# Optimization experiments

Measured on AMD Instinct MI355X. Metric: run time of the kernel, lower is better.

## Reference

```python
import jax, jax.numpy as jnp
import numpy as np
import math

BLOCK_SIZE = 512

def _block_attention(query, key, value):
    # query/key/value: [B, S, H, D]; block-wise attention with PER-BLOCK softmax
    # and normalizer accumulation, faithful to _ring_attention_single (causal, no dropout).
    B, S, H, D = query.shape
    bs = BLOCK_SIZE
    nb = S // bs
    scale = 1.0 / math.sqrt(D)
    neg = jnp.where(jnp.triu(jnp.ones((bs, bs), dtype=bool), 1), -jnp.inf, 0.0)  # strict-upper causal mask for diagonal block
    outs = []
    for i in range(nb):  # small fixed number of blocks (8)
        qb = query[:, i * bs:(i + 1) * bs]                      # [B, bs, H, D]
        kb = key[:, :(i + 1) * bs]                              # [B, (i+1)*bs, H, D]
        vb = value[:, :(i + 1) * bs].reshape(B, i + 1, bs, H, D)
        s = jnp.einsum('bqhd,bkhd->bhqk', qb, kb) * scale       # [B, H, bs, (i+1)*bs]
        s = s.reshape(B, H, bs, i + 1, bs)
        s = s.at[:, :, :, i, :].add(neg)                        # causal mask on diagonal block j == i
        p = jax.nn.softmax(s, axis=-1)                          # softmax PER kv block (faithful to source)
        o = jnp.einsum('bhqjk,bjkhd->bqhd', p, vb)              # accumulated block outputs
        norm = p.sum(axis=-1).sum(axis=-1)                      # [B, H, bs] accumulated normalizer (== i+1 per row)
        norm = jnp.clip(norm, 1e-6, None).transpose(0, 2, 1)[..., None]  # [B, bs, H, 1]
        outs.append(o / norm)
    return jnp.concatenate(outs, axis=1)  # [B, S, H, D]


def setup_inputs() -> dict:
    key = jax.random.key(0)
    k1, k2, k3 = jax.random.split(key, 3)
    shape = (2, 4096, 16, 128)
    return {
        'query': jax.random.normal(k1, shape, dtype=jnp.float32),
        'key': jax.random.normal(k2, shape, dtype=jnp.float32),
        'value': jax.random.normal(k3, shape, dtype=jnp.float32),
    }


def reference(query, key, value):
    return _block_attention(query, key, value)
```

## Files before the change

### kernel.cpp

```cpp
#include <hip/hip_runtime.h>

typedef short bf16x8 __attribute__((ext_vector_type(8)));
typedef short bf16x4 __attribute__((ext_vector_type(4)));
typedef float f32x4  __attribute__((ext_vector_type(4)));
typedef float f32x16 __attribute__((ext_vector_type(16)));
typedef unsigned int u32;
typedef u32 u32x4 __attribute__((ext_vector_type(4)));

#define SEQ 4096
#define NH  16
#define HD  128

__device__ __forceinline__ short bf16_rne(float x) {
  u32 u = __builtin_bit_cast(u32, x);
  u = (u + 0x7FFFu + ((u >> 16) & 1u)) >> 16;
  return (short)u;
}

typedef __attribute__((address_space(1))) const void as1c_void;
typedef __attribute__((address_space(3))) void as3_void;

#define CVTPK(d, a, b) asm("v_cvt_pk_bf16_f32 %0, %1, %2" : "=v"(d) : "v"(a), "v"(b))
#define PLSWAP(x, y)   asm("v_permlane32_swap_b32 %0, %1" : "+v"(x), "+v"(y))

__global__ __launch_bounds__(256) void prep_k(const float* __restrict__ K,
                                              short* __restrict__ Kp) {
  int idx = blockIdx.x * 256 + threadIdx.x;
  int d4 = idx & 31;
  int s  = (idx >> 5) & 4095;
  int h  = (idx >> 17) & 15;
  int b  = idx >> 21;
  f32x4 v = *(const f32x4*)(K + (((size_t)(b * SEQ + s) * NH + h) << 7) + d4 * 4);
  bf16x4 o;
  o[0] = bf16_rne(v[0]); o[1] = bf16_rne(v[1]);
  o[2] = bf16_rne(v[2]); o[3] = bf16_rne(v[3]);
  int x = (d4 * 4) ^ ((s & 7) << 3);
  *(bf16x4*)(Kp + (((size_t)(b * NH + h) * SEQ + s) << 7) + x) = o;
}

__global__ __launch_bounds__(256) void prep_v(const float* __restrict__ V,
                                              short* __restrict__ Vt) {
  __shared__ short tile[64 * 128];
  int bid = blockIdx.x;
  int sb = bid & 63;
  int h  = (bid >> 6) & 15;
  int b  = bid >> 10;
  int t = threadIdx.x;
  {
    int s = t >> 2;
    int dbase = (t & 3) * 32;
    const float* src = V + (((size_t)(b * SEQ + sb * 64 + s) * NH + h) << 7) + dbase;
    int sw = (s & 7) << 3;
#pragma unroll
    for (int j = 0; j < 8; ++j) {
      f32x4 v = *(const f32x4*)(src + j * 4);
      bf16x4 o;
      o[0] = bf16_rne(v[0]); o[1] = bf16_rne(v[1]);
      o[2] = bf16_rne(v[2]); o[3] = bf16_rne(v[3]);
      int d = dbase + j * 4;
      *(bf16x4*)&tile[s * 128 + (d ^ sw)] = o;
    }
  }
  __syncthreads();
  {
    int w = t >> 6, l = t & 63, g = l >> 4, lq = l & 15;
    int srel = lq * 4;
#pragma unroll
    for (int j = 0; j < 8; ++j) {
      int d = w * 32 + j * 4 + g;
      bf16x4 o;
#pragma unroll
      for (int i = 0; i < 4; ++i) {
        int s = srel + i;
        o[i] = tile[s * 128 + (d ^ ((s & 7) << 3))];
      }
      int sp = srel ^ ((d & 7) << 3);
      *(bf16x4*)(Vt + (((size_t)(b * NH + h) * HD + d) << 12) + sb * 64 + sp) = o;
    }
  }
}

__global__ __launch_bounds__(256, 2) void attn_main(const float* __restrict__ Q,
                                                    const short* __restrict__ Kp,
                                                    const short* __restrict__ Vt,
                                                    float* __restrict__ Out) {
  __shared__ __align__(16) short sK[2][64 * 128];
  __shared__ __align__(16) short sV[2][128 * 64];

  int bid0 = (int)blockIdx.x;
  int bid = (bid0 & 7) * 64 + (bid0 >> 3);
  int p  = bid & 15;
  int h  = (bid >> 4) & 15;
  int b  = bid >> 8;

  int tid = threadIdx.x;
  int l = tid & 63, w = tid >> 6;
  int q5 = l & 31;
  int hi = l >> 5;
  int hi4 = hi * 4, hi8 = hi * 8;
  int cswz = (l & 7) << 4;

  int kcol[8], vcol[4];
#pragma unroll
  for (int i = 0; i < 8; ++i) kcol[i] = (i * 32 + hi * 16) ^ cswz;
#pragma unroll
  for (int ks = 0; ks < 4; ++ks) vcol[ks] = (ks * 32 + hi * 16) ^ cswz;

  const int pat[16] = {0,1,2,3, 8,9,10,11, 16,17,18,19, 24,25,26,27};

  const char* KbB = (const char*)(Kp + ((size_t)(b * NH + h) << 19));
  const char* VbB = (const char*)(Vt + ((size_t)(b * NH + h) << 19));

  const char* kgb[4]; const char* vgb[4]; int ldo[4];
#pragma unroll
  for (int j = 0; j < 4; ++j) {
    int idx = j * 256 + tid;
    kgb[j] = KbB + idx * 16;
    vgb[j] = VbB + (size_t)(idx >> 3) * 8192 + (idx & 7) * 16;
    ldo[j] = idx * 16;
  }

  const float SCL = 0.08838834764831845f * 1.4426950408889634f;

  for (int ts = 0; ts < 2; ++ts) {
    int qt = ts ? p : (31 - p);
    int iblk = qt >> 2;
    int qrow0 = qt * 128 + w * 32;
    int qg = qrow0 + q5;
    int qgrel = (qt & 3) * 128 + w * 32 + q5;
    int nch_w = (qt & 3) * 2 + (w >> 1) + 1;
    int ntot = 8 * iblk + (qt & 3) * 2 + 2;

    bf16x8 qf[8];
    {
      const float* qp = Q + (((size_t)(b * SEQ + qg) * NH + h) << 7);
#pragma unroll
      for (int i = 0; i < 8; ++i) {
        int d0 = i * 16 + hi8;
        f32x4 a = *(const f32x4*)(qp + d0);
        f32x4 c2 = *(const f32x4*)(qp + d0 + 4);
        bf16x8 f;
        f[0] = bf16_rne(a[0] * SCL);  f[1] = bf16_rne(a[1] * SCL);
        f[2] = bf16_rne(a[2] * SCL);  f[3] = bf16_rne(a[3] * SCL);
        f[4] = bf16_rne(c2[0] * SCL); f[5] = bf16_rne(c2[1] * SCL);
        f[6] = bf16_rne(c2[2] * SCL); f[7] = bf16_rne(c2[3] * SCL);
        qf[i] = f;
      }
    }

    f32x16 ot[4], ob[4];
#pragma unroll
    for (int dt = 0; dt < 4; ++dt) {
#pragma unroll
      for (int r = 0; r < 16; ++r) { ot[dt][r] = 0.f; ob[dt][r] = 0.f; }
    }
    float Z = 0.0f;

    __syncthreads();
#pragma unroll
    for (int j = 0; j < 4; ++j) {
      __builtin_amdgcn_global_load_lds((as1c_void*)kgb[j], (as3_void*)((char*)sK[0] + ldo[j]), 16, 0, 0);
      __builtin_amdgcn_global_load_lds((as1c_void*)vgb[j], (as3_void*)((char*)sV[0] + ldo[j]), 16, 0, 0);
    }

#pragma unroll 2
    for (int t = 0; t < ntot; ++t) {
      __syncthreads();

      if (t + 1 < ntot) {
        int bi = (t + 1) & 1;
#pragma unroll
        for (int j = 0; j < 4; ++j) {
          __builtin_amdgcn_global_load_lds((as1c_void*)(kgb[j] + (size_t)(t + 1) * 16384),
                                           (as3_void*)((char*)sK[bi] + ldo[j]), 16, 0, 0);
          __builtin_amdgcn_global_load_lds((as1c_void*)(vgb[j] + (size_t)(t + 1) * 128),
                                           (as3_void*)((char*)sV[bi] + ldo[j]), 16, 0, 0);
        }
      }

      int jb = t >> 3, c = t & 7;
      const int diag = (jb == iblk);

      if (!(diag && c >= nch_w)) {
        const char* kbuf = (const char*)sK[t & 1];
        const char* vbuf = (const char*)sV[t & 1];
        bf16x8 pa[4];
        float csum = 0.0f;

#pragma unroll
        for (int kt = 0; kt < 2; ++kt) {
          f32x16 st;
#pragma unroll
          for (int r = 0; r < 16; ++r) st[r] = 0.f;
          int rowb = kt * 8192 + q5 * 256;
          __builtin_amdgcn_s_setprio(1);
#pragma unroll
          for (int i = 0; i < 8; ++i) {
            bf16x8 kf = *(const bf16x8*)(kbuf + rowb + kcol[i]);
            st = __builtin_amdgcn_mfma_f32_32x32x16_bf16(kf, qf[i], st, 0, 0, 0);
          }
          __builtin_amdgcn_s_setprio(0);

          if (diag && c == nch_w - 1) {
            int lim = qgrel - (c * 64 + kt * 32);
#pragma unroll
            for (int r = 0; r < 16; ++r) {
              if (pat[r] + hi4 > lim) st[r] = -1e30f;
            }
          }

          float pr[16];
#pragma unroll
          for (int r = 0; r < 16; ++r) {
            pr[r] = __builtin_amdgcn_exp2f(st[r]);
            csum += pr[r];
          }
          u32 X0, X1, Y0, Y1;
          CVTPK(X0, pr[0], pr[1]); CVTPK(X1, pr[2], pr[3]);
          CVTPK(Y0, pr[4], pr[5]); CVTPK(Y1, pr[6], pr[7]);
          PLSWAP(X0, Y0); PLSWAP(X1, Y1);
          pa[kt * 2] = __builtin_bit_cast(bf16x8, (u32x4){X0, X1, Y0, Y1});
          u32 A0, A1, B0, B1;
          CVTPK(A0, pr[8], pr[9]);   CVTPK(A1, pr[10], pr[11]);
          CVTPK(B0, pr[12], pr[13]); CVTPK(B1, pr[14], pr[15]);
          PLSWAP(A0, B0); PLSWAP(A1, B1);
          pa[kt * 2 + 1] = __builtin_bit_cast(bf16x8, (u32x4){A0, A1, B0, B1});
        }
        Z += csum;

        __builtin_amdgcn_s_setprio(1);
#pragma unroll
        for (int ks = 0; ks < 4; ++ks) {
#pragma unroll
          for (int dt = 0; dt < 4; ++dt) {
            bf16x8 vf = *(const bf16x8*)(vbuf + (dt * 32 + q5) * 128 + vcol[ks]);
            ob[dt] = __builtin_amdgcn_mfma_f32_32x32x16_bf16(pa[ks], vf, ob[dt], 0, 0, 0);
          }
        }
        __builtin_amdgcn_s_setprio(0);
      }

      if ((t & 7) == 7 || t == ntot - 1) {
        float zf = Z + __shfl_xor(Z, 32, 64);
        float rz[16];
#pragma unroll
        for (int r = 0; r < 16; ++r) rz[r] = 1.0f / __shfl(zf, pat[r] + hi4, 64);
#pragma unroll
        for (int dt = 0; dt < 4; ++dt) {
#pragma unroll
          for (int r = 0; r < 16; ++r) {
            ot[dt][r] += ob[dt][r] * rz[r];
            ob[dt][r] = 0.f;
          }
        }
        Z = 0.0f;
      }
    }

    float rnorm = 1.0f / (float)(iblk + 1);
#pragma unroll
    for (int dt = 0; dt < 4; ++dt) {
#pragma unroll
      for (int r = 0; r < 16; ++r) {
        int qrow = qrow0 + pat[r] + hi4;
        Out[(((size_t)(b * SEQ + qrow) * NH + h) << 7) + dt * 32 + q5] = ot[dt][r] * rnorm;
      }
    }
  }
}

extern "C" void kernel_launch(void* const* d_in, const int* in_sizes, int n_in,
                              void* d_out, int out_size, void* d_ws, size_t ws_size,
                              hipStream_t stream) {
  const float* Q = (const float*)d_in[0];
  const float* K = (const float*)d_in[1];
  const float* V = (const float*)d_in[2];
  float* out = (float*)d_out;

  short* Kp = (short*)d_ws;
  short* Vt = Kp + (size_t)2 * NH * SEQ * HD;

  prep_k<<<(2 * NH * SEQ * (HD / 4)) / 256, 256, 0, stream>>>(K, Kp);
  prep_v<<<2 * NH * (SEQ / 64), 256, 0, stream>>>(V, Vt);
  attn_main<<<2 * NH * 16, 256, 0, stream>>>(Q, Kp, Vt, out);
}
```

Measured before the change: 212.1 us.

## Split V prefetch after QK MFMAs and interleave softmax with PV MFMAs

Issues the next tile's K load first and defers the V global-to-LDS load until after the QK^T MFMAs, spreading memory traffic across the iteration. Computes both 32-row score tiles up front, then interleaves the exp/convert of each half with its PV MFMAs, so VALU softmax work can overlap matrix-core work. Also computes the reciprocal once per lane before the shuffle instead of sixteen divides. The cost is higher register pressure from holding two score accumulators live at once.

```diff
diff --git a/kernel.cpp b/kernel.cpp
--- a/kernel.cpp
+++ b/kernel.cpp
@@ -167,15 +167,13 @@
     for (int t = 0; t < ntot; ++t) {
       __syncthreads();
 
-      if (t + 1 < ntot) {
-        int bi = (t + 1) & 1;
-#pragma unroll
-        for (int j = 0; j < 4; ++j) {
+      int bi = (t + 1) & 1;
+      const int more = (t + 1 < ntot);
+      if (more) {
+#pragma unroll
+        for (int j = 0; j < 4; ++j)
           __builtin_amdgcn_global_load_lds((as1c_void*)(kgb[j] + (size_t)(t + 1) * 16384),
                                            (as3_void*)((char*)sK[bi] + ldo[j]), 16, 0, 0);
-          __builtin_amdgcn_global_load_lds((as1c_void*)(vgb[j] + (size_t)(t + 1) * 128),
-                                           (as3_void*)((char*)sV[bi] + ldo[j]), 16, 0, 0);
-        }
       }
 
       int jb = t >> 3, c = t & 7;
@@ -184,67 +182,118 @@
       if (!(diag && c >= nch_w)) {
         const char* kbuf = (const char*)sK[t & 1];
         const char* vbuf = (const char*)sV[t & 1];
-        bf16x8 pa[4];
         float csum = 0.0f;
 
-#pragma unroll
-        for (int kt = 0; kt < 2; ++kt) {
-          f32x16 st;
-#pragma unroll
-          for (int r = 0; r < 16; ++r) st[r] = 0.f;
-          int rowb = kt * 8192 + q5 * 256;
-          __builtin_amdgcn_s_setprio(1);
-#pragma unroll
-          for (int i = 0; i < 8; ++i) {
-            bf16x8 kf = *(const bf16x8*)(kbuf + rowb + kcol[i]);
-            st = __builtin_amdgcn_mfma_f32_32x32x16_bf16(kf, qf[i], st, 0, 0, 0);
+        f32x16 st0, st1;
+#pragma unroll
+        for (int r = 0; r < 16; ++r) { st0[r] = 0.f; st1[r] = 0.f; }
+        int rowb = q5 * 256;
+        __builtin_amdgcn_s_setprio(1);
+#pragma unroll
+        for (int i = 0; i < 8; ++i) {
+          bf16x8 kf = *(const bf16x8*)(kbuf + rowb + kcol[i]);
+          st0 = __builtin_amdgcn_mfma_f32_32x32x16_bf16(kf, qf[i], st0, 0, 0, 0);
+        }
+#pragma unroll
+        for (int i = 0; i < 8; ++i) {
+          bf16x8 kf = *(const bf16x8*)(kbuf + 8192 + rowb + kcol[i]);
+          st1 = __builtin_amdgcn_mfma_f32_32x32x16_bf16(kf, qf[i], st1, 0, 0, 0);
+        }
+        __builtin_amdgcn_s_setprio(0);
+
+        if (more) {
+#pragma unroll
+          for (int j = 0; j < 4; ++j)
+            __builtin_amdgcn_global_load_lds((as1c_void*)(vgb[j] + (size_t)(t + 1) * 128),
+                                             (as3_void*)((char*)sV[bi] + ldo[j]), 16, 0, 0);
+        }
+
+        if (diag && c == nch_w - 1) {
+          int lim0 = qgrel - c * 64;
+          int lim1 = lim0 - 32;
+#pragma unroll
+          for (int r = 0; r < 16; ++r) {
+            int pr4 = pat[r] + hi4;
+            if (pr4 > lim0) st0[r] = -1e30f;
+            if (pr4 > lim1) st1[r] = -1e30f;
           }
-          __builtin_amdgcn_s_setprio(0);
-
-          if (diag && c == nch_w - 1) {
-            int lim = qgrel - (c * 64 + kt * 32);
-#pragma unroll
-            for (int r = 0; r < 16; ++r) {
-              if (pat[r] + hi4 > lim) st[r] = -1e30f;
-            }
-          }
-
+        }
+
+        bf16x8 pa0, pa1, pa2, pa3;
+        {
           float pr[16];
 #pragma unroll
           for (int r = 0; r < 16; ++r) {
-            pr[r] = __builtin_amdgcn_exp2f(st[r]);
+            pr[r] = __builtin_amdgcn_exp2f(st0[r]);
             csum += pr[r];
           }
-          u32 X0, X1, Y0, Y1;
-          CVTPK(X0, pr[0], pr[1]); CVTPK(X1, pr[2], pr[3]);
-          CVTPK(Y0, pr[4], pr[5]); CVTPK(Y1, pr[6], pr[7]);
+          u32 X0, X1, Y0, Y1, A0, A1, B0, B1;
+          CVTPK(X0, pr[0], pr[1]);   CVTPK(X1, pr[2], pr[3]);
+          CVTPK(Y0, pr[4], pr[5]);   CVTPK(Y1, pr[6], pr[7]);
           PLSWAP(X0, Y0); PLSWAP(X1, Y1);
-          pa[kt * 2] = __builtin_bit_cast(bf16x8, (u32x4){X0, X1, Y0, Y1});
-          u32 A0, A1, B0, B1;
+          pa0 = __builtin_bit_cast(bf16x8, (u32x4){X0, X1, Y0, Y1});
           CVTPK(A0, pr[8], pr[9]);   CVTPK(A1, pr[10], pr[11]);
           CVTPK(B0, pr[12], pr[13]); CVTPK(B1, pr[14], pr[15]);
           PLSWAP(A0, B0); PLSWAP(A1, B1);
-          pa[kt * 2 + 1] = __builtin_bit_cast(bf16x8, (u32x4){A0, A1, B0, B1});
-        }
+          pa1 = __builtin_bit_cast(bf16x8, (u32x4){A0, A1, B0, B1});
+        }
+        __builtin_amdgcn_s_setprio(1);
+#pragma unroll
+        for (int dt = 0; dt < 4; ++dt) {
+          bf16x8 vf = *(const bf16x8*)(vbuf + (dt * 32 + q5) * 128 + vcol[0]);
+          ob[dt] = __builtin_amdgcn_mfma_f32_32x32x16_bf16(pa0, vf, ob[dt], 0, 0, 0);
+        }
+#pragma unroll
+        for (int dt = 0; dt < 4; ++dt) {
+          bf16x8 vf = *(const bf16x8*)(vbuf + (dt * 32 + q5) * 128 + vcol[1]);
+          ob[dt] = __builtin_amdgcn_mfma_f32_32x32x16_bf16(pa1, vf, ob[dt], 0, 0, 0);
+        }
+        __builtin_amdgcn_s_setprio(0);
+
+        {
+          float pr[16];
+#pragma unroll
+          for (int r = 0; r < 16; ++r) {
+            pr[r] = __builtin_amdgcn_exp2f(st1[r]);
+            csum += pr[r];
+          }
+          u32 X0, X1, Y0, Y1, A0, A1, B0, B1;
+          CVTPK(X0, pr[0], pr[1]);   CVTPK(X1, pr[2], pr[3]);
+          CVTPK(Y0, pr[4], pr[5]);   CVTPK(Y1, pr[6], pr[7]);
+          PLSWAP(X0, Y0); PLSWAP(X1, Y1);
+          pa2 = __builtin_bit_cast(bf16x8, (u32x4){X0, X1, Y0, Y1});
+          CVTPK(A0, pr[8], pr[9]);   CVTPK(A1, pr[10], pr[11]);
+          CVTPK(B0, pr[12], pr[13]); CVTPK(B1, pr[14], pr[15]);
+          PLSWAP(A0, B0); PLSWAP(A1, B1);
+          pa3 = __builtin_bit_cast(bf16x8, (u32x4){A0, A1, B0, B1});
+        }
+        __builtin_amdgcn_s_setprio(1);
+#pragma unroll
+        for (int dt = 0; dt < 4; ++dt) {
+          bf16x8 vf = *(const bf16x8*)(vbuf + (dt * 32 + q5) * 128 + vcol[2]);
+          ob[dt] = __builtin_amdgcn_mfma_f32_32x32x16_bf16(pa2, vf, ob[dt], 0, 0, 0);
+        }
+#pragma unroll
+        for (int dt = 0; dt < 4; ++dt) {
+          bf16x8 vf = *(const bf16x8*)(vbuf + (dt * 32 + q5) * 128 + vcol[3]);
+          ob[dt] = __builtin_amdgcn_mfma_f32_32x32x16_bf16(pa3, vf, ob[dt], 0, 0, 0);
+        }
+        __builtin_amdgcn_s_setprio(0);
+
         Z += csum;
-
-        __builtin_amdgcn_s_setprio(1);
-#pragma unroll
-        for (int ks = 0; ks < 4; ++ks) {
-#pragma unroll
-          for (int dt = 0; dt < 4; ++dt) {
-            bf16x8 vf = *(const bf16x8*)(vbuf + (dt * 32 + q5) * 128 + vcol[ks]);
-            ob[dt] = __builtin_amdgcn_mfma_f32_32x32x16_bf16(pa[ks], vf, ob[dt], 0, 0, 0);
-          }
-        }
-        __builtin_amdgcn_s_setprio(0);
+      } else if (more) {
+#pragma unroll
+        for (int j = 0; j < 4; ++j)
+          __builtin_amdgcn_global_load_lds((as1c_void*)(vgb[j] + (size_t)(t + 1) * 128),
+                                           (as3_void*)((char*)sV[bi] + ldo[j]), 16, 0, 0);
       }
 
       if ((t & 7) == 7 || t == ntot - 1) {
         float zf = Z + __shfl_xor(Z, 32, 64);
+        float rzL = 1.0f / zf;
         float rz[16];
 #pragma unroll
-        for (int r = 0; r < 16; ++r) rz[r] = 1.0f / __shfl(zf, pat[r] + hi4, 64);
+        for (int r = 0; r < 16; ++r) rz[r] = __shfl(rzL, pat[r] + hi4, 64);
 #pragma unroll
         for (int dt = 0; dt < 4; ++dt) {
 #pragma unroll
```

Result: faster. 205.8 us (-3.0%).
